# Performance work log

Hardware: AMD Instinct MI355X
Metric: run time of the kernel (lower is better)

The kernel has to match this reference:

```python
import jax, jax.numpy as jnp
import numpy as np

DEPTH, DIM, HEADS, MLP_HID, POS_DIM, PROJ_DIM, NCLS, INP = 5, 128, 8, 256, 128, 128, 1000, 35
EPS = 1e-5

def _ln(x, g, b):
    m = x.mean(-1, keepdims=True)
    v = ((x - m) ** 2).mean(-1, keepdims=True)
    return (x - m) / jnp.sqrt(v + EPS) * g + b

def _gelu(x):
    return jax.nn.gelu(x, approximate=False)  # torch nn.GELU default (erf)

def setup_inputs() -> dict:
    key = jax.random.key(0)
    ks = iter(jax.random.split(key, 80))
    nxt = lambda: next(ks)
    B, N = 8, 1024
    w = lambda *s: (jax.random.normal(nxt(), s, jnp.float32) / np.sqrt(s[-2]).astype(np.float32))
    z = lambda *s: jnp.zeros(s, jnp.float32)
    o = lambda *s: jnp.ones(s, jnp.float32)
    node_feat = jax.random.normal(nxt(), (B, N, 3), jnp.float32)
    a = (jax.random.uniform(nxt(), (B, N, N)) < 0.01).astype(jnp.float32)
    adj = jnp.maximum(a, a.transpose(0, 2, 1))  # symmetric 0/1 adjacency
    lapl = jax.random.normal(nxt(), (B, N, 32), jnp.float32) * 0.1
    d = dict(
        node_feat=node_feat, adj=adj, lapl=lapl,
        cls_token=jax.random.normal(nxt(), (1, 1, DIM), jnp.float32),
        pe_w1=w(INP, 2 * INP), pe_b1=z(2 * INP),
        pe_w2=w(2 * INP, 2 * INP), pe_b2=z(2 * INP),
        pe_w3=w(2 * INP, 2 * INP), pe_b3=z(2 * INP),
        pe_lng=o(2 * INP), pe_lnb=z(2 * INP),
        pe_w4=w(2 * INP, POS_DIM), pe_b4=z(POS_DIM),
        blk_ln1_g=o(DEPTH, DIM), blk_ln1_b=z(DEPTH, DIM),
        blk_qkv_w=w(DEPTH, DIM, 3 * HEADS * DIM),
        blk_proj_w=w(DEPTH, HEADS * DIM, DIM), blk_proj_b=z(DEPTH, DIM),
        blk_gamma_w=jax.random.uniform(nxt(), (DEPTH, DIM, 2), jnp.float32) * 0.01,
        blk_gamma_b=z(DEPTH, 2),
        blk_ln2_g=o(DEPTH, DIM), blk_ln2_b=z(DEPTH, DIM),
        blk_mlp_w1=w(DEPTH, DIM, MLP_HID), blk_mlp_b1=z(DEPTH, MLP_HID),
        blk_mlp_w2=w(DEPTH, MLP_HID, DIM), blk_mlp_b2=z(DEPTH, DIM),
        head_lng=o(DIM), head_lnb=z(DIM), head_w=w(DIM, DIM), head_b=z(DIM),
        proj_w1=w(DIM, PROJ_DIM), proj_b1=z(PROJ_DIM),
        proj_w2=w(PROJ_DIM, PROJ_DIM), proj_b2=z(PROJ_DIM),
        proj_w3=w(PROJ_DIM, PROJ_DIM), proj_b3=z(PROJ_DIM),
        proj_lng=o(PROJ_DIM), proj_lnb=z(PROJ_DIM),
        proj_w4=w(PROJ_DIM, NCLS), proj_b4=z(NCLS),
    )
    return d

def reference(node_feat, adj, lapl, cls_token, pe_w1, pe_b1, pe_w2, pe_b2, pe_w3, pe_b3,
              pe_lng, pe_lnb, pe_w4, pe_b4, blk_ln1_g, blk_ln1_b, blk_qkv_w, blk_proj_w,
              blk_proj_b, blk_gamma_w, blk_gamma_b, blk_ln2_g, blk_ln2_b, blk_mlp_w1,
              blk_mlp_b1, blk_mlp_w2, blk_mlp_b2, head_lng, head_lnb, head_w, head_b,
              proj_w1, proj_b1, proj_w2, proj_b2, proj_w3, proj_b3, proj_lng, proj_lnb,
              proj_w4, proj_b4):
    B, N, _ = node_feat.shape
    M = N + 1
    # positional-encoding MLP on concatenated [node_feat | lapl] (inp_dim = 35)
    x = jnp.concatenate([node_feat, lapl], axis=2)
    x = _gelu(x @ pe_w1 + pe_b1)
    x = _gelu(x @ pe_w2 + pe_b2)
    x = _gelu(x @ pe_w3 + pe_b3)
    x = _ln(x, pe_lng, pe_lnb) @ pe_w4 + pe_b4  # [B,N,DIM]
    x = jnp.concatenate([jnp.broadcast_to(cls_token, (B, 1, DIM)), x], axis=1)  # [B,M,DIM]
    # adjacency with cls row/col, adj_cls[:,0,0] = 1
    adj_cls = jnp.zeros((B, M, M), x.dtype).at[:, 0, 0].set(1.0).at[:, 1:, 1:].set(adj)
    scale = DIM ** (-0.5)
    for i in range(DEPTH):
        h = _ln(x, blk_ln1_g[i], blk_ln1_b[i])
        qkv = (h @ blk_qkv_w[i]).reshape(B, M, 3, HEADS, DIM).transpose(2, 0, 3, 1, 4)
        q, k, v = qkv[0], qkv[1], qkv[2]  # each [B,H,M,D]
        attn = jnp.einsum('bhnd,bhmd->bhnm', q, k) * scale
        gamma = jnp.exp(h @ blk_gamma_w[i] + blk_gamma_b[i])  # [B,M,2], use_exp=True
        attn = gamma[:, None, :, 0:1] * attn + gamma[:, None, :, 1:2] * adj_cls[:, None]
        attn = jax.nn.softmax(attn, axis=-1)
        o = jnp.einsum('bhnm,bhmd->bhnd', attn, v).transpose(0, 2, 1, 3).reshape(B, M, HEADS * DIM)
        x = o @ blk_proj_w[i] + blk_proj_b[i] + h  # residual from normed input (as in source)
        h2 = _ln(x, blk_ln2_g[i], blk_ln2_b[i])
        x = _gelu(h2 @ blk_mlp_w1[i] + blk_mlp_b1[i]) @ blk_mlp_w2[i] + blk_mlp_b2[i] + h2
    c = x[:, 0]
    c = _ln(c, head_lng, head_lnb) @ head_w + head_b  # mlp_head
    p = _gelu(c @ proj_w1 + proj_b1)
    p = _gelu(p @ proj_w2 + proj_b2)
    p = _gelu(p @ proj_w3 + proj_b3)
    p = _ln(p, proj_lng, proj_lnb) @ proj_w4 + proj_b4
    return (c, p)
```

## Files before the change

kernel.cpp:

```cpp
#include <hip/hip_runtime.h>
#include <hip/hip_bf16.h>
#include <math.h>

#define NB 8
#define NSEQ 1024
#define M_ 1025
#define ROWS (NB * M_)
#define DIMC 128
#define NHEADS 8
#define QKV3 3072
#define PEROWS (NB * NSEQ)
#define ACS 1088

typedef __attribute__((ext_vector_type(8))) short bf16x8;
typedef __attribute__((ext_vector_type(4))) float f32x4;

__device__ __forceinline__ float gelu_f(float x) {
  return 0.5f * x * (1.f + erff(x * 0.70710678118654752440f));
}

__device__ __forceinline__ unsigned short f2bf(float f) {
  __hip_bfloat16 h = __float2bfloat16(f);
  return *reinterpret_cast<unsigned short*>(&h);
}

__device__ __forceinline__ float bf2f(unsigned short u) {
  union { unsigned int i; float f; } c;
  c.i = ((unsigned int)u) << 16;
  return c.f;
}

__global__ __launch_bounds__(128) void pe_fused_k(
    const float* __restrict__ nf, const float* __restrict__ lp,
    const float* __restrict__ w1, const float* __restrict__ b1,
    const float* __restrict__ w2, const float* __restrict__ b2,
    const float* __restrict__ w3, const float* __restrict__ b3,
    const float* __restrict__ lng, const float* __restrict__ lnb,
    const float* __restrict__ w4, const float* __restrict__ b4,
    float* __restrict__ x)
{
  __shared__ float sA[16][36];
  __shared__ float sB[16][72];
  __shared__ float sC[16][72];
  const int tid = threadIdx.x;
  const int r0 = blockIdx.x * 16;

  for (int i = tid; i < 16 * 35; i += 128) {
    const int r = i / 35, c = i - r * 35;
    const int gr = r0 + r;
    sA[r][c] = (c < 3) ? nf[(size_t)gr * 3 + c] : lp[(size_t)gr * 32 + (c - 3)];
  }
  __syncthreads();
  if (tid < 70) {
    float acc[16];
#pragma unroll
    for (int r = 0; r < 16; ++r) acc[r] = b1[tid];
    for (int k = 0; k < 35; ++k) {
      const float wv = w1[k * 70 + tid];
#pragma unroll
      for (int r = 0; r < 16; ++r) acc[r] = fmaf(sA[r][k], wv, acc[r]);
    }
#pragma unroll
    for (int r = 0; r < 16; ++r) sB[r][tid] = gelu_f(acc[r]);
  }
  __syncthreads();
  if (tid < 70) {
    float acc[16];
#pragma unroll
    for (int r = 0; r < 16; ++r) acc[r] = b2[tid];
    for (int k = 0; k < 70; ++k) {
      const float wv = w2[k * 70 + tid];
#pragma unroll
      for (int r = 0; r < 16; ++r) acc[r] = fmaf(sB[r][k], wv, acc[r]);
    }
#pragma unroll
    for (int r = 0; r < 16; ++r) sC[r][tid] = gelu_f(acc[r]);
  }
  __syncthreads();
  if (tid < 70) {
    float acc[16];
#pragma unroll
    for (int r = 0; r < 16; ++r) acc[r] = b3[tid];
    for (int k = 0; k < 70; ++k) {
      const float wv = w3[k * 70 + tid];
#pragma unroll
      for (int r = 0; r < 16; ++r) acc[r] = fmaf(sC[r][k], wv, acc[r]);
    }
#pragma unroll
    for (int r = 0; r < 16; ++r) sB[r][tid] = gelu_f(acc[r]);
  }
  __syncthreads();
  if (tid < 16) {
    float m = 0.f;
    for (int d = 0; d < 70; ++d) m += sB[tid][d];
    m *= (1.f / 70.f);
    float v = 0.f;
    for (int d = 0; d < 70; ++d) { const float t = sB[tid][d] - m; v += t * t; }
    const float inv = rsqrtf(v * (1.f / 70.f) + 1e-5f);
    for (int d = 0; d < 70; ++d) sB[tid][d] = (sB[tid][d] - m) * inv * lng[d] + lnb[d];
  }
  __syncthreads();
  {
    float acc[16];
#pragma unroll
    for (int r = 0; r < 16; ++r) acc[r] = b4[tid];
    for (int k = 0; k < 70; ++k) {
      const float wv = w4[k * 128 + tid];
#pragma unroll
      for (int r = 0; r < 16; ++r) acc[r] = fmaf(sB[r][k], wv, acc[r]);
    }
#pragma unroll
    for (int r = 0; r < 16; ++r) {
      const int gr = r0 + r;
      x[(size_t)(gr + gr / 1024 + 1) * DIMC + tid] = acc[r];
    }
  }
}

template<int ACT, int OBF, int RES>
__global__ __launch_bounds__(256) void mgemm_k(
    const unsigned short* __restrict__ Xb, const unsigned short* __restrict__ Wt,
    const float* __restrict__ bias, const float* __restrict__ res,
    void* __restrict__ outp, int rows, int K, int N)
{
  __shared__ unsigned short sX[64][72];
  __shared__ unsigned short sW[64][72];
  const int tid = threadIdx.x;
  const int w = tid >> 6, lane = tid & 63;
  const int col = lane & 15, quad = lane >> 4;
  const int r0 = blockIdx.x * 64, n0 = blockIdx.y * 64;
  const int lr = tid >> 2, lc = tid & 3;
  const int xrow = min(r0 + lr, rows - 1);
  const unsigned short* xsrc = Xb + (size_t)xrow * K + lc * 8;
  const unsigned short* wsrc = Wt + (size_t)(n0 + lr) * K + lc * 8;

  f32x4 acc[4];
#pragma unroll
  for (int t = 0; t < 4; ++t) acc[t] = (f32x4){0.f, 0.f, 0.f, 0.f};

  for (int k0 = 0; k0 < K; k0 += 64) {
    __syncthreads();
    *(uint4*)&sX[lr][lc * 8]      = *(const uint4*)(xsrc + k0);
    *(uint4*)&sX[lr][lc * 8 + 32] = *(const uint4*)(xsrc + k0 + 32);
    *(uint4*)&sW[lr][lc * 8]      = *(const uint4*)(wsrc + k0);
    *(uint4*)&sW[lr][lc * 8 + 32] = *(const uint4*)(wsrc + k0 + 32);
    __syncthreads();
    const bf16x8 aX0 = *(const bf16x8*)&sX[w * 16 + col][quad * 8];
    const bf16x8 aX1 = *(const bf16x8*)&sX[w * 16 + col][32 + quad * 8];
#pragma unroll
    for (int t = 0; t < 4; ++t) {
      const bf16x8 bW0 = *(const bf16x8*)&sW[t * 16 + col][quad * 8];
      const bf16x8 bW1 = *(const bf16x8*)&sW[t * 16 + col][32 + quad * 8];
      acc[t] = __builtin_amdgcn_mfma_f32_16x16x32_bf16(aX0, bW0, acc[t], 0, 0, 0);
      acc[t] = __builtin_amdgcn_mfma_f32_16x16x32_bf16(aX1, bW1, acc[t], 0, 0, 0);
    }
  }
  const int gr_base = r0 + w * 16 + quad * 4;
#pragma unroll
  for (int t = 0; t < 4; ++t) {
    const int n = n0 + t * 16 + col;
    const float bv = bias ? bias[n] : 0.f;
#pragma unroll
    for (int r = 0; r < 4; ++r) {
      const int gr = gr_base + r;
      if (gr < rows) {
        float v = acc[t][r] + bv;
        if (ACT) v = gelu_f(v);
        if (RES) v += res[(size_t)gr * N + n];
        if (OBF) ((unsigned short*)outp)[(size_t)gr * N + n] = f2bf(v);
        else     ((float*)outp)[(size_t)gr * N + n] = v;
      }
    }
  }
}

template<int OBF, int VT>
__global__ __launch_bounds__(256) void mgemm128_k(
    const unsigned short* __restrict__ Xb, const unsigned short* __restrict__ Wt,
    const float* __restrict__ bias, void* __restrict__ outp,
    unsigned short* __restrict__ vtp, int rows, int K, int N)
{
  __shared__ unsigned short sX[128][72];
  __shared__ unsigned short sW[128][72];
  const int tid = threadIdx.x;
  const int w = tid >> 6, lane = tid & 63;
  const int col = lane & 15, quad = lane >> 4;
  const int wr = w >> 1, wc = w & 1;
  const int r0 = blockIdx.x * 128, n0 = blockIdx.y * 128;

  f32x4 acc[4][4];
#pragma unroll
  for (int i = 0; i < 4; ++i)
#pragma unroll
    for (int j = 0; j < 4; ++j) acc[i][j] = (f32x4){0.f, 0.f, 0.f, 0.f};

  for (int k0 = 0; k0 < K; k0 += 64) {
    __syncthreads();
#pragma unroll
    for (int l = 0; l < 4; ++l) {
      const int idx = l * 256 + tid;
      const int row = idx >> 3, c = idx & 7;
      const int xrow = min(r0 + row, rows - 1);
      *(uint4*)&sX[row][c * 8] = *(const uint4*)(Xb + (size_t)xrow * K + k0 + c * 8);
      *(uint4*)&sW[row][c * 8] = *(const uint4*)(Wt + (size_t)(n0 + row) * K + k0 + c * 8);
    }
    __syncthreads();
    bf16x8 aX[4][2];
#pragma unroll
    for (int i = 0; i < 4; ++i) {
      aX[i][0] = *(const bf16x8*)&sX[wr * 64 + i * 16 + col][quad * 8];
      aX[i][1] = *(const bf16x8*)&sX[wr * 64 + i * 16 + col][32 + quad * 8];
    }
#pragma unroll
    for (int j = 0; j < 4; ++j) {
      const bf16x8 b0 = *(const bf16x8*)&sW[wc * 64 + j * 16 + col][quad * 8];
      const bf16x8 b1 = *(const bf16x8*)&sW[wc * 64 + j * 16 + col][32 + quad * 8];
#pragma unroll
      for (int i = 0; i < 4; ++i) {
        acc[i][j] = __builtin_amdgcn_mfma_f32_16x16x32_bf16(aX[i][0], b0, acc[i][j], 0, 0, 0);
        acc[i][j] = __builtin_amdgcn_mfma_f32_16x16x32_bf16(aX[i][1], b1, acc[i][j], 0, 0, 0);
      }
    }
  }
  const bool dovt = VT && (n0 >= 2048);
#pragma unroll
  for (int i = 0; i < 4; ++i) {
    const int gr_base = r0 + wr * 64 + i * 16 + quad * 4;
    int bb[4], mm[4];
    if (dovt) {
#pragma unroll
      for (int r = 0; r < 4; ++r) {
        const int gr = gr_base + r;
        bb[r] = gr / 1025;
        mm[r] = gr - bb[r] * 1025;
      }
    }
#pragma unroll
    for (int j = 0; j < 4; ++j) {
      const int n = n0 + wc * 64 + j * 16 + col;
      const float bv = bias ? bias[n] : 0.f;
      const int hh = (n - 2048) >> 7;
      const int d  = (n - 2048) & 127;
#pragma unroll
      for (int r = 0; r < 4; ++r) {
        const int gr = gr_base + r;
        if (gr < rows) {
          const float v = acc[i][j][r] + bv;
          const unsigned short bf = f2bf(v);
          if (OBF) ((unsigned short*)outp)[(size_t)gr * N + n] = bf;
          else     ((float*)outp)[(size_t)gr * N + n] = v;
          if (dovt) vtp[(((size_t)(bb[r] * NHEADS + hh) * DIMC + d) * ACS) + mm[r]] = bf;
        }
      }
    }
  }
}

__global__ __launch_bounds__(256) void ln_rows_k(
    const float* __restrict__ in, float* __restrict__ out,
    unsigned short* __restrict__ outb,
    const float* __restrict__ g, const float* __restrict__ b,
    const float* __restrict__ gw, const float* __restrict__ gb,
    float* __restrict__ gamout, int rows, int D)
{
  const int wv = (blockIdx.x * blockDim.x + threadIdx.x) >> 6;
  const int lane = threadIdx.x & 63;
  if (wv >= rows) return;
  const float* r = in + (size_t)wv * D;
  float s = 0.f;
  for (int d = lane; d < D; d += 64) s += r[d];
  for (int off = 32; off; off >>= 1) s += __shfl_down(s, off);
  const float mean = __shfl(s, 0) / (float)D;
  float v = 0.f;
  for (int d = lane; d < D; d += 64) { float t = r[d] - mean; v += t * t; }
  for (int off = 32; off; off >>= 1) v += __shfl_down(v, off);
  const float inv = rsqrtf(__shfl(v, 0) / (float)D + 1e-5f);
  float* orow = out + (size_t)wv * D;
  float a0 = 0.f, a1 = 0.f;
  for (int d = lane; d < D; d += 64) {
    const float o = (r[d] - mean) * inv * g[d] + b[d];
    orow[d] = o;
    if (outb) outb[(size_t)wv * D + d] = f2bf(o);
    if (gw) { a0 = fmaf(o, gw[2 * d], a0); a1 = fmaf(o, gw[2 * d + 1], a1); }
  }
  if (gw) {
    for (int off = 32; off; off >>= 1) { a0 += __shfl_down(a0, off); a1 += __shfl_down(a1, off); }
    if (lane == 0) {
      gamout[(size_t)wv * 2 + 0] = expf(a0 + gb[0]);
      gamout[(size_t)wv * 2 + 1] = expf(a1 + gb[1]);
    }
  }
}

__global__ __launch_bounds__(256) void adjp_k(const float* __restrict__ adj,
                                              unsigned long long* __restrict__ adjp)
{
  const int n = blockIdx.x;
  const int b = blockIdx.y;
  const int wv = threadIdx.x >> 6, lane = threadIdx.x & 63;
  for (int w = wv; w < 17; w += 4) {
    const int m = w * 64 + lane;
    float av = 0.f;
    if (n == 0) av = (m == 0) ? 1.f : 0.f;
    else if (m >= 1 && m <= NSEQ) av = adj[((size_t)b * NSEQ + (n - 1)) * NSEQ + (m - 1)];
    const unsigned long long mask = __ballot(av != 0.f);
    if (lane == 0) adjp[((size_t)b * M_ + n) * 17 + w] = mask;
  }
}

__global__ void wtrans_k(const float* __restrict__ W, unsigned short* __restrict__ Wt,
                         int K, int N)
{
  __shared__ float t[32][33];
  const int k0 = blockIdx.x * 32, n0 = blockIdx.y * 32;
  const float* Wd = W + (size_t)blockIdx.z * K * N;
  unsigned short* Wtd = Wt + (size_t)blockIdx.z * K * N;
  for (int i = threadIdx.y; i < 32; i += 8)
    t[i][threadIdx.x] = Wd[(size_t)(k0 + i) * N + n0 + threadIdx.x];
  __syncthreads();
  for (int i = threadIdx.y; i < 32; i += 8)
    Wtd[(size_t)(n0 + i) * K + k0 + threadIdx.x] = f2bf(t[threadIdx.x][i]);
}

__global__ __launch_bounds__(512) void attn_mfma_k(
    const unsigned short* __restrict__ qkv, const float* __restrict__ gamma,
    const unsigned long long* __restrict__ adjp, const unsigned short* __restrict__ vt,
    unsigned short* __restrict__ o)
{
  __shared__ unsigned short sK[64][136];
  __shared__ unsigned short sVt[128][72];
  __shared__ unsigned short sP[128][72];

  const int hh = blockIdx.x, qt = blockIdx.y, b = blockIdx.z;
  const int tid = threadIdx.x;
  const int w = tid >> 6;
  const int lane = tid & 63;
  const int col = lane & 15;
  const int quad = lane >> 4;
  const int n0 = qt * 128;
  const int qbase = n0 + w * 16;
  const float scale = 0.088388347648318447f;

  bf16x8 aQ[4];
  {
    const int qrow = min(qbase + col, 1024);
    const unsigned short* qp = qkv + ((size_t)(b * M_ + qrow)) * QKV3 + hh * DIMC + quad * 8;
#pragma unroll
    for (int c = 0; c < 4; ++c) aQ[c] = *(const bf16x8*)(qp + c * 32);
  }
  float g0[4], g1[4];
  size_t adjo[4];
#pragma unroll
  for (int r = 0; r < 4; ++r) {
    const int nc = min(qbase + quad * 4 + r, 1024);
    g0[r] = gamma[(size_t)(b * M_ + nc) * 2 + 0] * scale;
    g1[r] = gamma[(size_t)(b * M_ + nc) * 2 + 1];
    adjo[r] = ((size_t)b * M_ + nc) * 17;
  }

  float l_i[4] = {0.f, 0.f, 0.f, 0.f};
  f32x4 Oacc[8];
#pragma unroll
  for (int t = 0; t < 8; ++t) Oacc[t] = (f32x4){0.f, 0.f, 0.f, 0.f};

  const size_t vtbase = ((size_t)(b * NHEADS + hh)) * DIMC * ACS;

  for (int kt = 0; kt < 17; ++kt) {
    const int m0 = kt * 64;
    __syncthreads();
#pragma unroll
    for (int l = 0; l < 2; ++l) {
      const int idx = l * 512 + tid;
      {
        const int m = idx >> 4, c = idx & 15;
        const int gm = m0 + m;
        uint4 kv = make_uint4(0u, 0u, 0u, 0u);
        if (gm < M_) kv = *(const uint4*)(qkv + ((size_t)(b * M_ + gm)) * QKV3 + 1024 + hh * DIMC + c * 8);
        *(uint4*)&sK[m][c * 8] = kv;
      }
      {
        const int d = idx >> 3, mc = idx & 7;
        const uint4 vv = *(const uint4*)(vt + vtbase + (size_t)d * ACS + m0 + mc * 8);
        const int swc = mc ^ ((d >> 3) & 7);
        *(uint4*)&sVt[d][swc * 8] = vv;
      }
    }
    __syncthreads();

    unsigned long long mk[4];
#pragma unroll
    for (int r = 0; r < 4; ++r) mk[r] = adjp[adjo[r] + kt];

    f32x4 Sacc[4];
#pragma unroll
    for (int t = 0; t < 4; ++t) Sacc[t] = (f32x4){0.f, 0.f, 0.f, 0.f};
#pragma unroll
    for (int t = 0; t < 4; ++t) {
#pragma unroll
      for (int c = 0; c < 4; ++c) {
        const bf16x8 bK = *(const bf16x8*)&sK[t * 16 + col][c * 32 + quad * 8];
        Sacc[t] = __builtin_amdgcn_mfma_f32_16x16x32_bf16(aQ[c], bK, Sacc[t], 0, 0, 0);
      }
    }

#pragma unroll
    for (int t = 0; t < 4; ++t) {
      const int m = m0 + t * 16 + col;
      const bool mv = (m < M_);
      const int chb = t * 2 + (col >> 3);
      const int sh = t * 16 + col;
#pragma unroll
      for (int r = 0; r < 4; ++r) {
        const float bias = ((mk[r] >> sh) & 1ull) ? g1[r] : 0.f;
        const float s = fmaf(g0[r], Sacc[t][r], bias);
        const float pv = mv ? __expf(s) : 0.f;
        l_i[r] += pv;
        const int ql = w * 16 + quad * 4 + r;
        sP[ql][((chb ^ (ql & 7)) * 8) + (col & 7)] = f2bf(pv);
      }
    }

#pragma unroll
    for (int ch = 0; ch < 2; ++ch) {
      const int r0a = w * 16 + col;
      const bf16x8 aP = *(const bf16x8*)&sP[r0a][(((ch * 4 + quad) ^ (col & 7)) * 8)];
#pragma unroll
      for (int t = 0; t < 8; ++t) {
        const int pc = (ch * 4 + quad) ^ ((t * 2 + (col >> 3)) & 7);
        const bf16x8 bV = *(const bf16x8*)&sVt[t * 16 + col][pc * 8];
        Oacc[t] = __builtin_amdgcn_mfma_f32_16x16x32_bf16(aP, bV, Oacc[t], 0, 0, 0);
      }
    }
  }

#pragma unroll
  for (int r = 0; r < 4; ++r) {
    float s = l_i[r];
    s += __shfl_xor(s, 1);
    s += __shfl_xor(s, 2);
    s += __shfl_xor(s, 4);
    s += __shfl_xor(s, 8);
    const int n = qbase + quad * 4 + r;
    if (n < M_) {
      const float invl = 1.f / s;
      unsigned short* orow = o + ((size_t)(b * M_ + n)) * (NHEADS * DIMC) + hh * DIMC + col;
#pragma unroll
      for (int t = 0; t < 8; ++t) orow[t * 16] = f2bf(Oacc[t][r] * invl);
    }
  }
}

__global__ __launch_bounds__(256) void head_fused_k(
    const float* __restrict__ x,
    const float* __restrict__ hlg, const float* __restrict__ hlb,
    const float* __restrict__ hw, const float* __restrict__ hb,
    const float* __restrict__ pw1, const float* __restrict__ pb1,
    const float* __restrict__ pw2, const float* __restrict__ pb2,
    const float* __restrict__ pw3, const float* __restrict__ pb3,
    const float* __restrict__ plg, const float* __restrict__ plb,
    const float* __restrict__ pw4, const float* __restrict__ pb4,
    float* __restrict__ out_c, float* __restrict__ out_p)
{
  __shared__ float sA[8][128];
  __shared__ float sB[8][128];
  const int tid = threadIdx.x;

  for (int i = tid; i < 8 * 128; i += 256) {
    const int bb = i >> 7, d = i & 127;
    sA[bb][d] = x[(size_t)bb * M_ * DIMC + d];
  }
  __syncthreads();
  if (tid < 8) {
    float m = 0.f;
    for (int d = 0; d < 128; ++d) m += sA[tid][d];
    m *= (1.f / 128.f);
    float v = 0.f;
    for (int d = 0; d < 128; ++d) { const float t = sA[tid][d] - m; v += t * t; }
    const float inv = rsqrtf(v * (1.f / 128.f) + 1e-5f);
    for (int d = 0; d < 128; ++d) sA[tid][d] = (sA[tid][d] - m) * inv * hlg[d] + hlb[d];
  }
  __syncthreads();
  {
    const int j = tid & 127, rb = (tid >> 7) * 4;
    float acc[4];
#pragma unroll
    for (int r = 0; r < 4; ++r) acc[r] = hb[j];
    for (int k = 0; k < 128; ++k) {
      const float wv = hw[k * 128 + j];
#pragma unroll
      for (int r = 0; r < 4; ++r) acc[r] = fmaf(sA[rb + r][k], wv, acc[r]);
    }
#pragma unroll
    for (int r = 0; r < 4; ++r) { sB[rb + r][j] = acc[r]; out_c[(rb + r) * 128 + j] = acc[r]; }
  }
  __syncthreads();
  const float* Ws[3] = {pw1, pw2, pw3};
  const float* Bs[3] = {pb1, pb2, pb3};
  for (int s = 0; s < 3; ++s) {
    const float (*src)[128] = (s & 1) ? sA : sB;
    float (*dst)[128] = (s & 1) ? sB : sA;
    const int j = tid & 127, rb = (tid >> 7) * 4;
    float acc[4];
#pragma unroll
    for (int r = 0; r < 4; ++r) acc[r] = Bs[s][j];
    for (int k = 0; k < 128; ++k) {
      const float wv = Ws[s][k * 128 + j];
#pragma unroll
      for (int r = 0; r < 4; ++r) acc[r] = fmaf(src[rb + r][k], wv, acc[r]);
    }
#pragma unroll
    for (int r = 0; r < 4; ++r) dst[rb + r][j] = gelu_f(acc[r]);
    __syncthreads();
  }
  if (tid < 8) {
    float m = 0.f;
    for (int d = 0; d < 128; ++d) m += sA[tid][d];
    m *= (1.f / 128.f);
    float v = 0.f;
    for (int d = 0; d < 128; ++d) { const float t = sA[tid][d] - m; v += t * t; }
    const float inv = rsqrtf(v * (1.f / 128.f) + 1e-5f);
    for (int d = 0; d < 128; ++d) sA[tid][d] = (sA[tid][d] - m) * inv * plg[d] + plb[d];
  }
  __syncthreads();
  for (int j = tid; j < 1000; j += 256) {
    float acc[8];
#pragma unroll
    for (int bb = 0; bb < 8; ++bb) acc[bb] = pb4[j];
    for (int k = 0; k < 128; ++k) {
      const float wv = pw4[(size_t)k * 1000 + j];
#pragma unroll
      for (int bb = 0; bb < 8; ++bb) acc[bb] = fmaf(sA[bb][k], wv, acc[bb]);
    }
#pragma unroll
    for (int bb = 0; bb < 8; ++bb) out_p[bb * 1000 + j] = acc[bb];
  }
}

__global__ void fill_cls_k(const float* __restrict__ cls, float* __restrict__ x)
{
  x[(size_t)blockIdx.x * M_ * DIMC + threadIdx.x] = cls[threadIdx.x];
}

extern "C" void kernel_launch(void* const* d_in, const int* in_sizes, int n_in,
                              void* d_out, int out_size, void* d_ws, size_t ws_size,
                              hipStream_t stream)
{
  (void)in_sizes; (void)n_in; (void)out_size; (void)ws_size;
  const float* node_feat = (const float*)d_in[0];
  const float* adj       = (const float*)d_in[1];
  const float* lapl      = (const float*)d_in[2];
  const float* cls_token = (const float*)d_in[3];
  const float* pe_w1 = (const float*)d_in[4];
  const float* pe_b1 = (const float*)d_in[5];
  const float* pe_w2 = (const float*)d_in[6];
  const float* pe_b2 = (const float*)d_in[7];
  const float* pe_w3 = (const float*)d_in[8];
  const float* pe_b3 = (const float*)d_in[9];
  const float* pe_lng = (const float*)d_in[10];
  const float* pe_lnb = (const float*)d_in[11];
  const float* pe_w4 = (const float*)d_in[12];
  const float* pe_b4 = (const float*)d_in[13];
  const float* blk_ln1_g = (const float*)d_in[14];
  const float* blk_ln1_b = (const float*)d_in[15];
  const float* blk_qkv_w = (const float*)d_in[16];
  const float* blk_proj_w = (const float*)d_in[17];
  const float* blk_proj_b = (const float*)d_in[18];
  const float* blk_gamma_w = (const float*)d_in[19];
  const float* blk_gamma_b = (const float*)d_in[20];
  const float* blk_ln2_g = (const float*)d_in[21];
  const float* blk_ln2_b = (const float*)d_in[22];
  const float* blk_mlp_w1 = (const float*)d_in[23];
  const float* blk_mlp_b1 = (const float*)d_in[24];
  const float* blk_mlp_w2 = (const float*)d_in[25];
  const float* blk_mlp_b2 = (const float*)d_in[26];
  const float* head_lng = (const float*)d_in[27];
  const float* head_lnb = (const float*)d_in[28];
  const float* head_w = (const float*)d_in[29];
  const float* head_b = (const float*)d_in[30];
  const float* proj_w1 = (const float*)d_in[31];
  const float* proj_b1 = (const float*)d_in[32];
  const float* proj_w2 = (const float*)d_in[33];
  const float* proj_b2 = (const float*)d_in[34];
  const float* proj_w3 = (const float*)d_in[35];
  const float* proj_b3 = (const float*)d_in[36];
  const float* proj_lng = (const float*)d_in[37];
  const float* proj_lnb = (const float*)d_in[38];
  const float* proj_w4 = (const float*)d_in[39];
  const float* proj_b4 = (const float*)d_in[40];

  float* ws   = (float*)d_ws;
  float* x    = ws;
  float* h    = x + 1049600;
  float* gam  = h + 1049600;
  float* obuf = gam + 16400;
  unsigned short* obufb = (unsigned short*)obuf;
  unsigned short* hidb  = (unsigned short*)(obuf + 4198400);
  float* sm  = obuf + 5248000;
  unsigned short* hb   = (unsigned short*)(sm + 8192);
  unsigned short* qkv  = hb + 1049600;
  unsigned long long* adjp = (unsigned long long*)(qkv + 25190400);
  unsigned short* vt   = (unsigned short*)(adjp + 139400 + 88);
  unsigned short* qkvWt = vt + 8912896;
  unsigned short* projWt = qkvWt + 5 * 393216;
  unsigned short* mlp1Wt = projWt + 5 * 131072;
  unsigned short* mlp2Wt = mlp1Wt + 5 * 32768;

  float* out_c = (float*)d_out;
  float* out_p = out_c + NB * DIMC;

  adjp_k<<<dim3(M_, NB), 256, 0, stream>>>(adj, adjp);
  wtrans_k<<<dim3(4, 96, 5), dim3(32, 8), 0, stream>>>(blk_qkv_w, qkvWt, 128, 3072);
  wtrans_k<<<dim3(32, 4, 5), dim3(32, 8), 0, stream>>>(blk_proj_w, projWt, 1024, 128);
  wtrans_k<<<dim3(4, 8, 5), dim3(32, 8), 0, stream>>>(blk_mlp_w1, mlp1Wt, 128, 256);
  wtrans_k<<<dim3(8, 4, 5), dim3(32, 8), 0, stream>>>(blk_mlp_w2, mlp2Wt, 256, 128);

  pe_fused_k<<<512, 128, 0, stream>>>(node_feat, lapl, pe_w1, pe_b1, pe_w2, pe_b2,
                                      pe_w3, pe_b3, pe_lng, pe_lnb, pe_w4, pe_b4, x);
  fill_cls_k<<<NB, DIMC, 0, stream>>>(cls_token, x);

  const int lnGrid = (ROWS * 64 + 255) / 256;
  for (int i = 0; i < 5; ++i) {
    const float* ln1g = blk_ln1_g + i * DIMC;
    const float* ln1b = blk_ln1_b + i * DIMC;
    const float* pb   = blk_proj_b + i * DIMC;
    const float* gw   = blk_gamma_w + (size_t)i * DIMC * 2;
    const float* gb   = blk_gamma_b + i * 2;
    const float* ln2g = blk_ln2_g + i * DIMC;
    const float* ln2b = blk_ln2_b + i * DIMC;
    const float* mb1  = blk_mlp_b1 + i * 256;
    const float* mb2  = blk_mlp_b2 + i * DIMC;
    const unsigned short* qw = qkvWt + (size_t)i * 393216;
    const unsigned short* pw = projWt + (size_t)i * 131072;
    const unsigned short* m1w = mlp1Wt + (size_t)i * 32768;
    const unsigned short* m2w = mlp2Wt + (size_t)i * 32768;

    ln_rows_k<<<lnGrid, 256, 0, stream>>>(x, h, hb, ln1g, ln1b, gw, gb, gam, ROWS, DIMC);
    mgemm128_k<1, 1><<<dim3(65, 24), 256, 0, stream>>>(hb, qw, nullptr, qkv, vt, ROWS, 128, 3072);
    attn_mfma_k<<<dim3(NHEADS, 9, NB), 512, 0, stream>>>(qkv, gam, adjp, vt, obufb);
    mgemm_k<0, 0, 1><<<dim3(129, 2), 256, 0, stream>>>(obufb, pw, pb, h, x, ROWS, 1024, 128);
    ln_rows_k<<<lnGrid, 256, 0, stream>>>(x, h, hb, ln2g, ln2b, nullptr, nullptr, nullptr, ROWS, DIMC);
    mgemm_k<1, 1, 0><<<dim3(129, 4), 256, 0, stream>>>(hb, m1w, mb1, nullptr, hidb, ROWS, 128, 256);
    mgemm_k<0, 0, 1><<<dim3(129, 2), 256, 0, stream>>>(hidb, m2w, mb2, h, x, ROWS, 256, 128);
  }

  head_fused_k<<<1, 256, 0, stream>>>(x, head_lng, head_lnb, head_w, head_b,
                                      proj_w1, proj_b1, proj_w2, proj_b2,
                                      proj_w3, proj_b3, proj_lng, proj_lnb,
                                      proj_w4, proj_b4, out_c, out_p);
}
```

Measured before the change: 1.555 ms.

## Double-buffer K tiles with direct global-to-LDS loads in attention kernel

The attention kernel now stages K and V^T tiles with global_load_lds (direct global-to-LDS DMA) instead of loading through registers. K is double-buffered so the next tile loads during the current tile's work. V loads overlap the QK^T MFMA and softmax, and adjacency mask bits are prefetched one tile ahead. LDS padding is replaced by XOR swizzles, and s_setprio is raised around the MFMA blocks. Manual vmcnt waits and barriers replace the earlier syncthreads pairs, which adds risk of synchronization mistakes.

```diff
diff --git a/kernel.cpp b/kernel.cpp
--- a/kernel.cpp
+++ b/kernel.cpp
@@ -28,6 +28,12 @@
   union { unsigned int i; float f; } c;
   c.i = ((unsigned int)u) << 16;
   return c.f;
+}
+
+__device__ __forceinline__ void g2lds16(const void* g, void* l) {
+  __builtin_amdgcn_global_load_lds(
+      (__attribute__((address_space(1))) void*)(g),
+      (__attribute__((address_space(3))) void*)(l), 16, 0, 0);
 }
 
 __global__ __launch_bounds__(128) void pe_fused_k(
@@ -327,9 +333,9 @@
     const unsigned long long* __restrict__ adjp, const unsigned short* __restrict__ vt,
     unsigned short* __restrict__ o)
 {
-  __shared__ unsigned short sK[64][136];
-  __shared__ unsigned short sVt[128][72];
-  __shared__ unsigned short sP[128][72];
+  __shared__ unsigned short sK[2][64][128];
+  __shared__ unsigned short sVt[128][64];
+  __shared__ unsigned short sP[128][64];
 
   const int hh = blockIdx.x, qt = blockIdx.y, b = blockIdx.z;
   const int tid = threadIdx.x;
@@ -365,43 +371,53 @@
 
   const size_t vtbase = ((size_t)(b * NHEADS + hh)) * DIMC * ACS;
 
+  auto stageK = [&](int buf, int kt_) {
+#pragma unroll
+    for (int l = 0; l < 2; ++l) {
+      const int m = l * 32 + w * 4 + (lane >> 4);
+      const int gm = min(kt_ * 64 + m, 1024);
+      const unsigned short* src = qkv + ((size_t)(b * M_ + gm)) * QKV3 + 1024
+                                  + hh * DIMC + (((lane & 15) ^ (m & 7)) * 8);
+      g2lds16(src, &sK[buf][l * 32 + w * 4][0]);
+    }
+  };
+  auto stageV = [&](int kt_) {
+#pragma unroll
+    for (int l = 0; l < 2; ++l) {
+      const int d = l * 64 + w * 8 + (lane >> 3);
+      const unsigned short* src = vt + vtbase + (size_t)d * ACS + kt_ * 64
+                                  + (((lane & 7) ^ (d & 7)) * 8);
+      g2lds16(src, &sVt[l * 64 + w * 8][0]);
+    }
+  };
+
+  stageK(0, 0);
+  unsigned long long mk[4];
+#pragma unroll
+  for (int r = 0; r < 4; ++r) mk[r] = adjp[adjo[r] + 0];
+
+  int cur = 0;
   for (int kt = 0; kt < 17; ++kt) {
     const int m0 = kt * 64;
     __syncthreads();
-#pragma unroll
-    for (int l = 0; l < 2; ++l) {
-      const int idx = l * 512 + tid;
-      {
-        const int m = idx >> 4, c = idx & 15;
-        const int gm = m0 + m;
-        uint4 kv = make_uint4(0u, 0u, 0u, 0u);
-        if (gm < M_) kv = *(const uint4*)(qkv + ((size_t)(b * M_ + gm)) * QKV3 + 1024 + hh * DIMC + c * 8);
-        *(uint4*)&sK[m][c * 8] = kv;
-      }
-      {
-        const int d = idx >> 3, mc = idx & 7;
-        const uint4 vv = *(const uint4*)(vt + vtbase + (size_t)d * ACS + m0 + mc * 8);
-        const int swc = mc ^ ((d >> 3) & 7);
-        *(uint4*)&sVt[d][swc * 8] = vv;
-      }
-    }
-    __syncthreads();
-
-    unsigned long long mk[4];
-#pragma unroll
-    for (int r = 0; r < 4; ++r) mk[r] = adjp[adjo[r] + kt];
+
+    stageV(kt);
+    const bool more = (kt < 16);
+    if (more) stageK(cur ^ 1, kt + 1);
 
     f32x4 Sacc[4];
 #pragma unroll
     for (int t = 0; t < 4; ++t) Sacc[t] = (f32x4){0.f, 0.f, 0.f, 0.f};
+    __builtin_amdgcn_s_setprio(1);
 #pragma unroll
     for (int t = 0; t < 4; ++t) {
 #pragma unroll
       for (int c = 0; c < 4; ++c) {
-        const bf16x8 bK = *(const bf16x8*)&sK[t * 16 + col][c * 32 + quad * 8];
+        const bf16x8 bK = *(const bf16x8*)&sK[cur][t * 16 + col][((c * 4 + quad) ^ (col & 7)) * 8];
         Sacc[t] = __builtin_amdgcn_mfma_f32_16x16x32_bf16(aQ[c], bK, Sacc[t], 0, 0, 0);
       }
     }
+    __builtin_amdgcn_s_setprio(0);
 
 #pragma unroll
     for (int t = 0; t < 4; ++t) {
@@ -420,17 +436,29 @@
       }
     }
 
+    if (more) asm volatile("s_waitcnt vmcnt(2)" ::: "memory");
+    else      asm volatile("s_waitcnt vmcnt(0)" ::: "memory");
+    __builtin_amdgcn_s_barrier();
+    __builtin_amdgcn_sched_barrier(0);
+
+    if (more) {
+#pragma unroll
+      for (int r = 0; r < 4; ++r) mk[r] = adjp[adjo[r] + kt + 1];
+    }
+
+    __builtin_amdgcn_s_setprio(1);
 #pragma unroll
     for (int ch = 0; ch < 2; ++ch) {
-      const int r0a = w * 16 + col;
-      const bf16x8 aP = *(const bf16x8*)&sP[r0a][(((ch * 4 + quad) ^ (col & 7)) * 8)];
+      const int pr = w * 16 + col;
+      const bf16x8 aP = *(const bf16x8*)&sP[pr][((ch * 4 + quad) ^ (col & 7)) * 8];
 #pragma unroll
       for (int t = 0; t < 8; ++t) {
-        const int pc = (ch * 4 + quad) ^ ((t * 2 + (col >> 3)) & 7);
-        const bf16x8 bV = *(const bf16x8*)&sVt[t * 16 + col][pc * 8];
+        const bf16x8 bV = *(const bf16x8*)&sVt[t * 16 + col][((ch * 4 + quad) ^ (col & 7)) * 8];
         Oacc[t] = __builtin_amdgcn_mfma_f32_16x16x32_bf16(aP, bV, Oacc[t], 0, 0, 0);
       }
     }
+    __builtin_amdgcn_s_setprio(0);
+    cur ^= 1;
   }
 
 #pragma unroll
```

After: 1.452 ms. -6.7%, faster.
